# Optimization experiments

Hardware: AMD Instinct MI355X
Metric: run time of the kernel (lower is better)

Reference implementation:

```python
import jax, jax.numpy as jnp
import numpy as np


def setup_inputs() -> dict:
    key = jax.random.key(0)
    kq, ks, kr, kx, ky = jax.random.split(key, 5)
    B, C, H, W, K = 2, 64, 128, 256, 32
    Q = jax.random.normal(kq, (B, C, H, W), dtype=jnp.float32)
    S = jax.random.normal(ks, (B, C, H, W), dtype=jnp.float32)
    R = jax.random.normal(kr, (B, C, H, W), dtype=jnp.float32)
    Pos_x = jax.random.randint(kx, (H * W, K), 0, H, dtype=jnp.int64 if jax.config.jax_enable_x64 else jnp.int32)
    Pos_y = jax.random.randint(ky, (H * W, K), 0, W, dtype=jnp.int64 if jax.config.jax_enable_x64 else jnp.int32)
    return {"Q": Q, "S": S, "R": R, "Pos_x": Pos_x, "Pos_y": Pos_y}


def reference(Q, S, R, Pos_x, Pos_y):
    B, C, H, W = Q.shape
    N = H * W
    px = Pos_x.reshape(-1)  # [N*K]
    py = Pos_y.reshape(-1)
    K = px.shape[0] // N
    # Gather keys/values at candidate positions: [B, C, N*K] -> [B, C, N, K]
    Key = S[:, :, px, py].reshape(B, C, N, K)
    Value = R[:, :, px, py].reshape(B, C, N, K)
    # Queries: [B, N, C]
    Qf = Q.reshape(B, C, N).transpose(0, 2, 1)
    # Per-pixel scores over K candidates (NO 1/sqrt(d) scaling, as in original)
    score = jnp.einsum('bnc,bcnk->bnk', Qf, Key)
    attn = jax.nn.softmax(score, axis=-1)
    # Attention-weighted sum of values: [B, N, C]
    out = jnp.einsum('bnk,bcnk->bnc', attn, Value)
    return out.reshape(B, H, W, C).transpose(0, 3, 1, 2)
```

## Files before the change

### kernel.cpp

```cpp
#include <hip/hip_runtime.h>
#include <hip/hip_fp16.h>

constexpr int B = 2, C = 64, H = 128, W = 256, N = H * W, K = 32;

typedef _Float16 hf2 __attribute__((ext_vector_type(2)));

template <int CTRL>
__device__ __forceinline__ float dppf(float x) {
    int i = __builtin_bit_cast(int, x);
    int r = __builtin_amdgcn_update_dpp(i, i, CTRL, 0xF, 0xF, false);
    return __builtin_bit_cast(float, r);
}

__global__ __launch_bounds__(256) void fepam_prep(
    const float* __restrict__ Q, const float* __restrict__ S,
    const float* __restrict__ R,
    const int* __restrict__ Px, const int* __restrict__ Py,
    __half* __restrict__ Qt, __half* __restrict__ St, __half* __restrict__ Rt,
    unsigned short* __restrict__ Idx) {
    const int n0 = blockIdx.x * 64;
    const int b  = blockIdx.y;
    const int z  = blockIdx.z;

    if (z == 3) {
        if (b) return;
#pragma unroll
        for (int t = 0; t < 8; ++t) {
            const int e  = threadIdx.x + 256 * t;
            const int nl = e >> 5, k = e & 31;
            const int n  = n0 + nl;
            const int idx = Px[(size_t)n * K + k] * W + Py[(size_t)n * K + k];
            Idx[(size_t)n * K + (k & 7) * 4 + (k >> 3)] = (unsigned short)idx;
        }
        return;
    }

    __shared__ float tile[C][65];
    const float* src = (z == 0 ? S : (z == 1 ? R : Q)) + (size_t)b * C * N;
    __half2* d2 = (__half2*)((z == 0 ? St : (z == 1 ? Rt : Qt)) +
                             (size_t)b * N * C);
    {
        const int j = threadIdx.x & 63, c0 = threadIdx.x >> 6;
        const float* s = src + n0 + j;
#pragma unroll
        for (int r = 0; r < 16; ++r) {
            int c = c0 + r * 4;
            tile[c][j] = s[(size_t)c * N];
        }
    }
    __syncthreads();
    {
        const int c2 = threadIdx.x & 31, j0 = threadIdx.x >> 5;
#pragma unroll
        for (int r = 0; r < 8; ++r) {
            int j = j0 + 8 * r;
            d2[(size_t)(n0 + j) * 32 + c2] =
                __floats2half2_rn(tile[2 * c2][j], tile[2 * c2 + 1][j]);
        }
    }
}

__global__ __launch_bounds__(256, 6) void fepam_scores(
    const __half* __restrict__ Qt, const unsigned short* __restrict__ Idx,
    const __half* __restrict__ St, __half* __restrict__ Attn) {
    const int tid  = threadIdx.x;
    const int lane = tid & 63;
    const int wave = tid >> 6;
    const int bx   = blockIdx.x;
    const int b    = bx & 1;
    const int n0   = (bx >> 1) * 32;

    const int c_oct = lane & 7;
    const int k_loc = lane >> 3;

    const __half* Qtb = Qt + (size_t)b * N * C;
    const __half* Stb = St + (size_t)b * N * C;
    __half* AttnB = Attn + (size_t)b * N * K;

#pragma unroll
    for (int p = 0; p < 8; ++p) {
        const int n = n0 + wave * 8 + p;

        const ushort4 iv = *(const ushort4*)(Idx + (size_t)n * K + k_loc * 4);
        const float4 qraw = *(const float4*)(Qtb + (size_t)n * C + c_oct * 8);
        const int idxg[4] = {iv.x, iv.y, iv.z, iv.w};

        float s[4];
#pragma unroll
        for (int g = 0; g < 4; ++g) {
            const float4 kraw =
                *(const float4*)(Stb + ((size_t)idxg[g] << 6) + c_oct * 8);
            const hf2* k2 = (const hf2*)&kraw;
            const hf2* q2 = (const hf2*)&qraw;
            float acc = 0.f;
#pragma unroll
            for (int u = 0; u < 4; ++u)
                acc = __builtin_amdgcn_fdot2(k2[u], q2[u], acc, false);
            s[g] = acc;
        }
#pragma unroll
        for (int g = 0; g < 4; ++g) {
            s[g] += dppf<0xB1>(s[g]);
            s[g] += dppf<0x4E>(s[g]);
            s[g] += dppf<0x141>(s[g]);
        }

        float m = fmaxf(fmaxf(s[0], s[1]), fmaxf(s[2], s[3]));
        m = fmaxf(m, dppf<0x128>(m));
        m = fmaxf(m, __shfl_xor(m, 16));
        m = fmaxf(m, __shfl_xor(m, 32));
        float e0 = __expf(s[0] - m), e1 = __expf(s[1] - m);
        float e2 = __expf(s[2] - m), e3 = __expf(s[3] - m);
        float l = (e0 + e1) + (e2 + e3);
        l += dppf<0x128>(l);
        l += __shfl_xor(l, 16);
        l += __shfl_xor(l, 32);
        const float inv = 1.0f / l;

        if (c_oct == 0) {
            ushort4 av;
            av.x = __half_as_ushort(__float2half_rn(e0 * inv));
            av.y = __half_as_ushort(__float2half_rn(e1 * inv));
            av.z = __half_as_ushort(__float2half_rn(e2 * inv));
            av.w = __half_as_ushort(__float2half_rn(e3 * inv));
            *(ushort4*)(AttnB + (size_t)n * K + k_loc * 4) = av;
        }
    }
}

__global__ __launch_bounds__(256, 6) void fepam_values(
    const unsigned short* __restrict__ Idx, const __half* __restrict__ Attn,
    const __half* __restrict__ Rt, float* __restrict__ Out) {
    __shared__ __align__(16) float ot[32][66];

    const int tid  = threadIdx.x;
    const int lane = tid & 63;
    const int wave = tid >> 6;
    const int bx   = blockIdx.x;
    const int b    = bx & 1;
    const int n0   = (bx >> 1) * 32;

    const int c_oct = lane & 7;
    const int k_loc = lane >> 3;
    const bool hi8  = (lane & 8)  != 0;
    const bool hi16 = (lane & 16) != 0;
    const bool hi32 = (lane & 32) != 0;

    const __half* Rtb = Rt + (size_t)b * N * C;
    const __half* AttnB = Attn + (size_t)b * N * K;

#pragma unroll
    for (int p = 0; p < 8; ++p) {
        const int j = wave * 8 + p;
        const int n = n0 + j;

        const ushort4 iv = *(const ushort4*)(Idx + (size_t)n * K + k_loc * 4);
        const ushort4 av = *(const ushort4*)(AttnB + (size_t)n * K + k_loc * 4);
        const int idxg[4] = {iv.x, iv.y, iv.z, iv.w};
        const float a[4] = {__half2float(__ushort_as_half(av.x)),
                            __half2float(__ushort_as_half(av.y)),
                            __half2float(__ushort_as_half(av.z)),
                            __half2float(__ushort_as_half(av.w))};

        float acc[8] = {0, 0, 0, 0, 0, 0, 0, 0};
#pragma unroll
        for (int g = 0; g < 4; ++g) {
            const float4 vraw =
                *(const float4*)(Rtb + ((size_t)idxg[g] << 6) + c_oct * 8);
            const __half2* v2 = (const __half2*)&vraw;
#pragma unroll
            for (int u = 0; u < 4; ++u) {
                const float2 vf = __half22float2(v2[u]);
                acc[2 * u]     = fmaf(a[g], vf.x, acc[2 * u]);
                acc[2 * u + 1] = fmaf(a[g], vf.y, acc[2 * u + 1]);
            }
        }

        float r4[4];
#pragma unroll
        for (int i = 0; i < 4; ++i) {
            const float send = hi8 ? acc[i] : acc[4 + i];
            const float recv = dppf<0x128>(send);
            r4[i] = (hi8 ? acc[4 + i] : acc[i]) + recv;
        }
        float r2[2];
#pragma unroll
        for (int i = 0; i < 2; ++i) {
            const float send = hi16 ? r4[i] : r4[2 + i];
            const float recv = __shfl_xor(send, 16);
            r2[i] = (hi16 ? r4[2 + i] : r4[i]) + recv;
        }
        {
            const float send = hi32 ? r2[0] : r2[1];
            const float recv = __shfl_xor(send, 32);
            const float r1   = (hi32 ? r2[1] : r2[0]) + recv;
            const int c = c_oct * 8 + (hi8 ? 4 : 0) + (hi16 ? 2 : 0) + (hi32 ? 1 : 0);
            ot[j][c] = r1;
        }
    }
    __syncthreads();

    {
        const int j = tid & 31, c0 = tid >> 5;
        float* od = Out + (size_t)b * C * N + n0 + j;
#pragma unroll
        for (int r = 0; r < 8; ++r) {
            int c = c0 + r * 8;
            od[(size_t)c * N] = ot[j][c];
        }
    }
}

extern "C" void kernel_launch(void* const* d_in, const int* in_sizes, int n_in,
                              void* d_out, int out_size, void* d_ws, size_t ws_size,
                              hipStream_t stream) {
    const float* Q  = (const float*)d_in[0];
    const float* S  = (const float*)d_in[1];
    const float* R  = (const float*)d_in[2];
    const int*   Px = (const int*)d_in[3];
    const int*   Py = (const int*)d_in[4];
    float* Out = (float*)d_out;

    __half* St = (__half*)d_ws;
    __half* Rt = St + (size_t)B * N * C;
    __half* Qt = Rt + (size_t)B * N * C;
    unsigned short* Idx = (unsigned short*)(Qt + (size_t)B * N * C);
    __half* Attn = (__half*)(Idx + (size_t)N * K);

    dim3 pgrid(N / 64, B, 4);
    fepam_prep<<<pgrid, 256, 0, stream>>>(Q, S, R, Px, Py, Qt, St, Rt, Idx);

    dim3 ggrid(N / 32 * B);
    fepam_scores<<<ggrid, 256, 0, stream>>>(Qt, Idx, St, Attn);
    fepam_values<<<ggrid, 256, 0, stream>>>(Idx, Attn, Rt, Out);
}
```

Measured before the change: 139.9 us.

## Software-pipeline gathers and pack index with attention weight in one word

Both the scores and values kernels now prefetch the next pixel's gathered key/value rows and the index/query two pixels ahead, so the dependent-gather latency overlaps with the current pixel's compute. The scores kernel writes a packed 32-bit word holding the gather index in the high half and the fp16 attention weight in the low half. The values kernel therefore reads one uint4 instead of separate index and attention loads. This raises register pressure under the 6-waves-per-SIMD launch bound and doubles the size of the attention buffer written and read.

```diff
diff --git a/kernel.cpp b/kernel.cpp
--- a/kernel.cpp
+++ b/kernel.cpp
@@ -10,6 +10,13 @@
     int i = __builtin_bit_cast(int, x);
     int r = __builtin_amdgcn_update_dpp(i, i, CTRL, 0xF, 0xF, false);
     return __builtin_bit_cast(float, r);
+}
+
+__device__ __forceinline__ unsigned sel4(const uint4& v, int g) {
+    return g == 0 ? v.x : g == 1 ? v.y : g == 2 ? v.z : v.w;
+}
+__device__ __forceinline__ unsigned sel4(const ushort4& v, int g) {
+    return g == 0 ? v.x : g == 1 ? v.y : g == 2 ? v.z : v.w;
 }
 
 __global__ __launch_bounds__(256) void fepam_prep(
@@ -62,36 +69,53 @@
 
 __global__ __launch_bounds__(256, 6) void fepam_scores(
     const __half* __restrict__ Qt, const unsigned short* __restrict__ Idx,
-    const __half* __restrict__ St, __half* __restrict__ Attn) {
+    const __half* __restrict__ St, unsigned* __restrict__ AI) {
     const int tid  = threadIdx.x;
     const int lane = tid & 63;
     const int wave = tid >> 6;
     const int bx   = blockIdx.x;
     const int b    = bx & 1;
-    const int n0   = (bx >> 1) * 32;
+    const int n0   = (bx >> 1) * 32 + wave * 8;
 
     const int c_oct = lane & 7;
     const int k_loc = lane >> 3;
 
     const __half* Qtb = Qt + (size_t)b * N * C;
     const __half* Stb = St + (size_t)b * N * C;
-    __half* AttnB = Attn + (size_t)b * N * K;
+    unsigned* AIb = AI + (size_t)b * N * K;
+
+    auto ldi = [&](int p) {
+        return *(const ushort4*)(Idx + (size_t)(n0 + p) * K + k_loc * 4);
+    };
+    auto ldq = [&](int p) {
+        return *(const float4*)(Qtb + (size_t)(n0 + p) * C + c_oct * 8);
+    };
+    auto ldk = [&](const ushort4& iv, int g) {
+        return *(const float4*)(Stb + ((size_t)sel4(iv, g) << 6) + c_oct * 8);
+    };
+
+    ushort4 iv_c = ldi(0), iv_n = ldi(1);
+    float4  q_c  = ldq(0), q_n  = ldq(1);
+    float4  k_c[4];
+#pragma unroll
+    for (int g = 0; g < 4; ++g) k_c[g] = ldk(iv_c, g);
 
 #pragma unroll
     for (int p = 0; p < 8; ++p) {
-        const int n = n0 + wave * 8 + p;
-
-        const ushort4 iv = *(const ushort4*)(Idx + (size_t)n * K + k_loc * 4);
-        const float4 qraw = *(const float4*)(Qtb + (size_t)n * C + c_oct * 8);
-        const int idxg[4] = {iv.x, iv.y, iv.z, iv.w};
+        float4 k_n[4];
+        if (p < 7) {
+#pragma unroll
+            for (int g = 0; g < 4; ++g) k_n[g] = ldk(iv_n, g);
+        }
+        ushort4 iv_2;
+        float4  q_2;
+        if (p < 6) { iv_2 = ldi(p + 2); q_2 = ldq(p + 2); }
 
         float s[4];
 #pragma unroll
         for (int g = 0; g < 4; ++g) {
-            const float4 kraw =
-                *(const float4*)(Stb + ((size_t)idxg[g] << 6) + c_oct * 8);
-            const hf2* k2 = (const hf2*)&kraw;
-            const hf2* q2 = (const hf2*)&qraw;
+            const hf2* k2 = (const hf2*)&k_c[g];
+            const hf2* q2 = (const hf2*)&q_c;
             float acc = 0.f;
 #pragma unroll
             for (int u = 0; u < 4; ++u)
@@ -104,7 +128,6 @@
             s[g] += dppf<0x4E>(s[g]);
             s[g] += dppf<0x141>(s[g]);
         }
-
         float m = fmaxf(fmaxf(s[0], s[1]), fmaxf(s[2], s[3]));
         m = fmaxf(m, dppf<0x128>(m));
         m = fmaxf(m, __shfl_xor(m, 16));
@@ -118,19 +141,28 @@
         const float inv = 1.0f / l;
 
         if (c_oct == 0) {
-            ushort4 av;
-            av.x = __half_as_ushort(__float2half_rn(e0 * inv));
-            av.y = __half_as_ushort(__float2half_rn(e1 * inv));
-            av.z = __half_as_ushort(__float2half_rn(e2 * inv));
-            av.w = __half_as_ushort(__float2half_rn(e3 * inv));
-            *(ushort4*)(AttnB + (size_t)n * K + k_loc * 4) = av;
-        }
+            uint4 wv;
+            wv.x = ((unsigned)iv_c.x << 16) |
+                   __half_as_ushort(__float2half_rn(e0 * inv));
+            wv.y = ((unsigned)iv_c.y << 16) |
+                   __half_as_ushort(__float2half_rn(e1 * inv));
+            wv.z = ((unsigned)iv_c.z << 16) |
+                   __half_as_ushort(__float2half_rn(e2 * inv));
+            wv.w = ((unsigned)iv_c.w << 16) |
+                   __half_as_ushort(__float2half_rn(e3 * inv));
+            *(uint4*)(AIb + (size_t)(n0 + p) * K + k_loc * 4) = wv;
+        }
+
+#pragma unroll
+        for (int g = 0; g < 4; ++g) k_c[g] = k_n[g];
+        iv_c = iv_n; q_c = q_n;
+        iv_n = iv_2; q_n = q_2;
     }
 }
 
 __global__ __launch_bounds__(256, 6) void fepam_values(
-    const unsigned short* __restrict__ Idx, const __half* __restrict__ Attn,
-    const __half* __restrict__ Rt, float* __restrict__ Out) {
+    const unsigned* __restrict__ AI, const __half* __restrict__ Rt,
+    float* __restrict__ Out) {
     __shared__ __align__(16) float ot[32][66];
 
     const int tid  = threadIdx.x;
@@ -138,7 +170,8 @@
     const int wave = tid >> 6;
     const int bx   = blockIdx.x;
     const int b    = bx & 1;
-    const int n0   = (bx >> 1) * 32;
+    const int n0t  = (bx >> 1) * 32;
+    const int n0   = n0t + wave * 8;
 
     const int c_oct = lane & 7;
     const int k_loc = lane >> 3;
@@ -147,27 +180,40 @@
     const bool hi32 = (lane & 32) != 0;
 
     const __half* Rtb = Rt + (size_t)b * N * C;
-    const __half* AttnB = Attn + (size_t)b * N * K;
+    const unsigned* AIb = AI + (size_t)b * N * K;
+
+    auto ldw = [&](int p) {
+        return *(const uint4*)(AIb + (size_t)(n0 + p) * K + k_loc * 4);
+    };
+    auto ldv = [&](const uint4& wv, int g) {
+        return *(const float4*)(Rtb + ((size_t)(sel4(wv, g) >> 16) << 6) +
+                                c_oct * 8);
+    };
+
+    uint4  w_c = ldw(0), w_n = ldw(1);
+    float4 v_c[4];
+#pragma unroll
+    for (int g = 0; g < 4; ++g) v_c[g] = ldv(w_c, g);
 
 #pragma unroll
     for (int p = 0; p < 8; ++p) {
-        const int j = wave * 8 + p;
-        const int n = n0 + j;
-
-        const ushort4 iv = *(const ushort4*)(Idx + (size_t)n * K + k_loc * 4);
-        const ushort4 av = *(const ushort4*)(AttnB + (size_t)n * K + k_loc * 4);
-        const int idxg[4] = {iv.x, iv.y, iv.z, iv.w};
-        const float a[4] = {__half2float(__ushort_as_half(av.x)),
-                            __half2float(__ushort_as_half(av.y)),
-                            __half2float(__ushort_as_half(av.z)),
-                            __half2float(__ushort_as_half(av.w))};
-
+        float4 v_n[4];
+        if (p < 7) {
+#pragma unroll
+            for (int g = 0; g < 4; ++g) v_n[g] = ldv(w_n, g);
+        }
+        uint4 w_2;
+        if (p < 6) w_2 = ldw(p + 2);
+
+        const float a[4] = {
+            __half2float(__ushort_as_half((unsigned short)(w_c.x & 0xffffu))),
+            __half2float(__ushort_as_half((unsigned short)(w_c.y & 0xffffu))),
+            __half2float(__ushort_as_half((unsigned short)(w_c.z & 0xffffu))),
+            __half2float(__ushort_as_half((unsigned short)(w_c.w & 0xffffu)))};
         float acc[8] = {0, 0, 0, 0, 0, 0, 0, 0};
 #pragma unroll
         for (int g = 0; g < 4; ++g) {
-            const float4 vraw =
-                *(const float4*)(Rtb + ((size_t)idxg[g] << 6) + c_oct * 8);
-            const __half2* v2 = (const __half2*)&vraw;
+            const __half2* v2 = (const __half2*)&v_c[g];
 #pragma unroll
             for (int u = 0; u < 4; ++u) {
                 const float2 vf = __half22float2(v2[u]);
@@ -195,14 +241,19 @@
             const float recv = __shfl_xor(send, 32);
             const float r1   = (hi32 ? r2[1] : r2[0]) + recv;
             const int c = c_oct * 8 + (hi8 ? 4 : 0) + (hi16 ? 2 : 0) + (hi32 ? 1 : 0);
-            ot[j][c] = r1;
-        }
+            ot[wave * 8 + p][c] = r1;
+        }
+
+#pragma unroll
+        for (int g = 0; g < 4; ++g) v_c[g] = v_n[g];
+        w_c = w_n;
+        w_n = w_2;
     }
     __syncthreads();
 
     {
         const int j = tid & 31, c0 = tid >> 5;
-        float* od = Out + (size_t)b * C * N + n0 + j;
+        float* od = Out + (size_t)b * C * N + n0t + j;
 #pragma unroll
         for (int r = 0; r < 8; ++r) {
             int c = c0 + r * 8;
@@ -225,12 +276,12 @@
     __half* Rt = St + (size_t)B * N * C;
     __half* Qt = Rt + (size_t)B * N * C;
     unsigned short* Idx = (unsigned short*)(Qt + (size_t)B * N * C);
-    __half* Attn = (__half*)(Idx + (size_t)N * K);
+    unsigned* AI = (unsigned*)(Idx + (size_t)N * K);
 
     dim3 pgrid(N / 64, B, 4);
     fepam_prep<<<pgrid, 256, 0, stream>>>(Q, S, R, Px, Py, Qt, St, Rt, Idx);
 
     dim3 ggrid(N / 32 * B);
-    fepam_scores<<<ggrid, 256, 0, stream>>>(Qt, Idx, St, Attn);
-    fepam_values<<<ggrid, 256, 0, stream>>>(Idx, Attn, Rt, Out);
-}
+    fepam_scores<<<ggrid, 256, 0, stream>>>(Qt, Idx, St, AI);
+    fepam_values<<<ggrid, 256, 0, stream>>>(AI, Rt, Out);
+}
```

Result: no change. 137.2 us (-1.9%).
